# Kernel tuning notes

Hardware: AMD Instinct MI355X
Metric: run time of the kernel (lower is better)

## Reference

```python
import jax, jax.numpy as jnp
import numpy as np

B, T, D, HD = 4, 4096, 1024, 64

def setup_inputs() -> dict:
    key = jax.random.key(0)
    k1, k2, k3, k4 = jax.random.split(key, 4)
    scale = 1.0 / np.sqrt(D)
    return {
        "x": jax.random.normal(k1, (B, T, D), dtype=jnp.float32),
        "Wq": jax.random.normal(k2, (HD, D), dtype=jnp.float32) * scale,
        "Wk": jax.random.normal(k3, (HD, D), dtype=jnp.float32) * scale,
        "Wv": jax.random.normal(k4, (HD, D), dtype=jnp.float32) * scale,
    }

def reference(x, Wq, Wk, Wv):
    # x: [B,T,D]; W*: [head_dim, D] (torch Linear weight layout)
    Q = jnp.einsum('btd,hd->bth', x, Wq)  # [B,T,HD]
    K = jnp.einsum('btd,hd->bth', x, Wk)
    V = jnp.einsum('btd,hd->bth', x, Wv)
    hd = Q.shape[-1]
    scores = jnp.einsum('bqh,bkh->bqk', Q, K) * (hd ** -0.5)  # [B,T,T]
    t = scores.shape[1]
    causal = jnp.tril(jnp.ones((t, t), dtype=bool))
    scores = jnp.where(causal, scores, -jnp.inf)
    att = jax.nn.softmax(scores, axis=-1)
    return jnp.einsum('bqk,bkh->bqh', att, V)  # [B,T,HD]
```

## Files before the change

kernel.cpp:

```cpp
#include <hip/hip_runtime.h>
#include <stdint.h>

#define B_  4
#define T_  4096
#define D_  1024
#define HD_ 64
#define BT_ 16384

typedef short bf16x8 __attribute__((ext_vector_type(8)));
typedef float f32x4  __attribute__((ext_vector_type(4)));
typedef unsigned short u16;
typedef u16 u16x4 __attribute__((ext_vector_type(4)));

#define M0_ 8.0f

__device__ __forceinline__ u16 f2bf(float f) {
    union { float f; unsigned u; } v; v.f = f;
    unsigned r = (v.u + 0x7FFF + ((v.u >> 16) & 1)) >> 16;
    return (u16)r;
}
__device__ __forceinline__ float bf2f(u16 u) {
    union { unsigned u; float f; } v; v.u = ((unsigned)u) << 16;
    return v.f;
}

__device__ __forceinline__ int slot_base(int qt) {
    int a = qt >> 4, r = qt & 15;
    return qt + 8 * a * (a - 1) + a * r;
}

__global__ __launch_bounds__(256) void wconv_kernel(
    const float* __restrict__ wq, const float* __restrict__ wk,
    const float* __restrict__ wv, u16* __restrict__ wb)
{
    const int j   = blockIdx.x >> 5;
    const int off = (blockIdx.x & 31) * 2048 + threadIdx.x * 8;
    const float* src = (j == 0) ? wq : ((j == 1) ? wk : wv);
    f32x4 a0 = *(const f32x4*)(src + off);
    f32x4 a1 = *(const f32x4*)(src + off + 4);
    bf16x8 b;
    #pragma unroll
    for (int i = 0; i < 4; ++i) { b[i] = (short)f2bf(a0[i]); b[4 + i] = (short)f2bf(a1[i]); }
    *(bf16x8*)(wb + j * 65536 + off) = b;
}

__global__ __launch_bounds__(256) void qkv_kernel(
    const float* __restrict__ x, const u16* __restrict__ wb,
    u16* __restrict__ qs, u16* __restrict__ kss, u16* __restrict__ vssT)
{
    __shared__ __align__(16) u16 xt[32][72];
    __shared__ __align__(16) u16 wt[192][72];

    const int tid  = threadIdx.x;
    const int lane = tid & 63;
    const int w    = tid >> 6;
    const int quad = lane >> 4;
    const int l16  = lane & 15;
    const int row0 = blockIdx.x * 32;
    const int sp   = w >> 1;
    const int gh   = (w & 1) * 6;

    const int xrow = tid >> 3;
    const int xcg  = tid & 7;

    f32x4 acc[6];
    #pragma unroll
    for (int g = 0; g < 6; ++g) acc[g] = (f32x4)0.0f;

    f32x4 xa, xb;
    bf16x8 wr[6];
    {
        const float* xp = x + (size_t)(row0 + xrow) * D_ + xcg * 8;
        xa = *(const f32x4*)xp; xb = *(const f32x4*)(xp + 4);
        #pragma unroll
        for (int i = 0; i < 6; ++i) {
            int chunk = tid + 256 * i;
            wr[i] = *(const bf16x8*)(wb + (size_t)(chunk >> 3) * D_ + (chunk & 7) * 8);
        }
    }

    for (int kc = 0; kc < 16; ++kc) {
        __syncthreads();
        {
            bf16x8 px;
            #pragma unroll
            for (int i = 0; i < 4; ++i) { px[i] = (short)f2bf(xa[i]); px[4 + i] = (short)f2bf(xb[i]); }
            *(bf16x8*)&xt[xrow][xcg * 8] = px;
            #pragma unroll
            for (int i = 0; i < 6; ++i) {
                int chunk = tid + 256 * i;
                *(bf16x8*)&wt[chunk >> 3][(chunk & 7) * 8] = wr[i];
            }
        }
        __syncthreads();
        if (kc < 15) {
            const float* xp = x + (size_t)(row0 + xrow) * D_ + (kc + 1) * 64 + xcg * 8;
            xa = *(const f32x4*)xp; xb = *(const f32x4*)(xp + 4);
            #pragma unroll
            for (int i = 0; i < 6; ++i) {
                int chunk = tid + 256 * i;
                wr[i] = *(const bf16x8*)(wb + (size_t)(chunk >> 3) * D_ + (kc + 1) * 64 + (chunk & 7) * 8);
            }
        }
        #pragma unroll
        for (int ks = 0; ks < 2; ++ks) {
            bf16x8 a = *(const bf16x8*)&xt[sp * 16 + l16][ks * 32 + quad * 8];
            #pragma unroll
            for (int g = 0; g < 6; ++g) {
                bf16x8 b = *(const bf16x8*)&wt[(gh + g) * 16 + l16][ks * 32 + quad * 8];
                acc[g] = __builtin_amdgcn_mfma_f32_16x16x32_bf16(a, b, acc[g], 0, 0, 0);
            }
        }
    }
    #pragma unroll
    for (int g = 0; g < 6; ++g) {
        const int n = (gh + g) * 16 + l16;
        const int j = n >> 6, h = n & 63;
        const int rbase = row0 + sp * 16 + quad * 4;
        if (j == 0) {
            #pragma unroll
            for (int r = 0; r < 4; ++r) qs[(size_t)(rbase + r) * HD_ + h] = f2bf(acc[g][r] * 0.125f);
        } else if (j == 1) {
            #pragma unroll
            for (int r = 0; r < 4; ++r) kss[(size_t)(rbase + r) * HD_ + h] = f2bf(acc[g][r]);
        } else {
            u16x4 v;
            #pragma unroll
            for (int r = 0; r < 4; ++r) v[r] = f2bf(acc[g][r]);
            *(u16x4*)(vssT + (size_t)h * BT_ + rbase) = v;
        }
    }
}

__global__ __launch_bounds__(256) void attn_kernel(
    const u16* __restrict__ qs, const u16* __restrict__ kss,
    const u16* __restrict__ vssT,
    float* __restrict__ pl, u16* __restrict__ pO)
{
    __shared__ __align__(16) u16 kt[64][72];
    __shared__ __align__(16) u16 vt[80][72];
    __shared__ __align__(16) u16 pt[4][16][72];

    const int bi = blockIdx.x;
    const int c  = bi & 3;
    const int qt = (bi >> 2) & 63;
    const int b  = bi >> 8;
    if ((c << 4) > qt) return;

    const int kt0  = c << 4;
    const int kend = ((kt0 + 15) < qt) ? (kt0 + 15) : qt;

    const int tid  = threadIdx.x;
    const int lane = tid & 63;
    const int w    = tid >> 6;
    const int quad = lane >> 4;
    const int l16  = lane & 15;
    const int qb   = qt * 64;
    const size_t base = (size_t)b * T_;

    for (int idx = tid; idx < 16 * 72; idx += 256) {
        int rr = idx / 72, cc = idx - rr * 72;
        vt[64 + rr][cc] = (rr == 0) ? (u16)0x3F80 : (u16)0;
    }

    bf16x8 qf[2];
    {
        const u16* qp = qs + (base + qb + w * 16 + l16) * HD_ + quad * 8;
        qf[0] = *(const bf16x8*)(qp);
        qf[1] = *(const bf16x8*)(qp + 32);
    }

    f32x4 o_acc[5];
    #pragma unroll
    for (int g = 0; g < 5; ++g) o_acc[g] = (f32x4)0.0f;

    const int lr = tid >> 2, lp = tid & 3;

    bf16x8 kr0, kr1, vr0, vr1;
    {
        const u16* sk = kss + (base + kt0 * 64 + lr) * HD_ + lp * 16;
        kr0 = *(const bf16x8*)(sk);  kr1 = *(const bf16x8*)(sk + 8);
        const u16* sv = vssT + (size_t)lr * BT_ + base + kt0 * 64 + lp * 16;
        vr0 = *(const bf16x8*)(sv);  vr1 = *(const bf16x8*)(sv + 8);
    }

    for (int kti = kt0; kti <= kend; ++kti) {
        __syncthreads();
        *(bf16x8*)&kt[lr][lp * 16]     = kr0;
        *(bf16x8*)&kt[lr][lp * 16 + 8] = kr1;
        *(bf16x8*)&vt[lr][lp * 16]     = vr0;
        *(bf16x8*)&vt[lr][lp * 16 + 8] = vr1;
        __syncthreads();
        if (kti < kend) {
            const u16* sk = kss + (base + (kti + 1) * 64 + lr) * HD_ + lp * 16;
            kr0 = *(const bf16x8*)(sk);  kr1 = *(const bf16x8*)(sk + 8);
            const u16* sv = vssT + (size_t)lr * BT_ + base + (kti + 1) * 64 + lp * 16;
            vr0 = *(const bf16x8*)(sv);  vr1 = *(const bf16x8*)(sv + 8);
        }

        f32x4 s[4];
        #pragma unroll
        for (int g = 0; g < 4; ++g) {
            s[g] = (f32x4)0.0f;
            #pragma unroll
            for (int ks = 0; ks < 2; ++ks) {
                bf16x8 kf = *(const bf16x8*)&kt[g * 16 + l16][ks * 32 + quad * 8];
                s[g] = __builtin_amdgcn_mfma_f32_16x16x32_bf16(qf[ks], kf, s[g], 0, 0, 0);
            }
        }
        if (kti == qt) {
            #pragma unroll
            for (int g = 0; g < 4; ++g) {
                int key = kti * 64 + g * 16 + l16;
                #pragma unroll
                for (int r = 0; r < 4; ++r) {
                    int q = qb + w * 16 + quad * 4 + r;
                    if (key > q) s[g][r] = -1e30f;
                }
            }
        }
        #pragma unroll
        for (int g = 0; g < 4; ++g)
            #pragma unroll
            for (int r = 0; r < 4; ++r)
                pt[w][quad * 4 + r][g * 16 + l16] = f2bf(__expf(s[g][r] - M0_));
        #pragma unroll
        for (int ks = 0; ks < 2; ++ks) {
            bf16x8 pa = *(const bf16x8*)&pt[w][l16][ks * 32 + quad * 8];
            #pragma unroll
            for (int g = 0; g < 5; ++g) {
                bf16x8 vf = *(const bf16x8*)&vt[g * 16 + l16][ks * 32 + quad * 8];
                o_acc[g] = __builtin_amdgcn_mfma_f32_16x16x32_bf16(pa, vf, o_acc[g], 0, 0, 0);
            }
        }
    }

    const int slot = b * 160 + slot_base(qt) + c;
    if (l16 == 0) {
        #pragma unroll
        for (int r = 0; r < 4; ++r)
            pl[slot * 64 + w * 16 + quad * 4 + r] = o_acc[4][r];
    }
    #pragma unroll
    for (int g = 0; g < 4; ++g) {
        #pragma unroll
        for (int r = 0; r < 4; ++r) {
            int row = w * 16 + quad * 4 + r;
            pO[(size_t)slot * 4096 + row * 64 + g * 16 + l16] = f2bf(o_acc[g][r]);
        }
    }
}

__global__ __launch_bounds__(256) void merge_kernel(
    const float* __restrict__ pl, const u16* __restrict__ pO,
    float* __restrict__ out)
{
    const int bi = blockIdx.x;
    const int qt = bi & 63, b = bi >> 6;
    const int nc = (qt >> 4) + 1;
    const int s0 = b * 160 + slot_base(qt);
    const int row = threadIdx.x >> 2;
    const int hg  = (threadIdx.x & 3) * 16;

    float L = 0.0f;
    for (int c2 = 0; c2 < nc; ++c2) L += pl[(s0 + c2) * 64 + row];

    float o[16];
    #pragma unroll
    for (int i = 0; i < 16; ++i) o[i] = 0.0f;
    for (int c2 = 0; c2 < nc; ++c2) {
        const u16* p = pO + (size_t)(s0 + c2) * 4096 + row * 64 + hg;
        bf16x8 v0 = *(const bf16x8*)p;
        bf16x8 v1 = *(const bf16x8*)(p + 8);
        #pragma unroll
        for (int i = 0; i < 8; ++i) {
            o[i]     += bf2f((u16)v0[i]);
            o[8 + i] += bf2f((u16)v1[i]);
        }
    }
    const float inv = 1.0f / L;
    float* op = out + ((size_t)b * T_ + qt * 64 + row) * HD_ + hg;
    #pragma unroll
    for (int j = 0; j < 4; ++j) {
        f32x4 v;
        #pragma unroll
        for (int i = 0; i < 4; ++i) v[i] = o[j * 4 + i] * inv;
        *(f32x4*)(op + j * 4) = v;
    }
}

extern "C" void kernel_launch(void* const* d_in, const int* in_sizes, int n_in,
                              void* d_out, int out_size, void* d_ws, size_t ws_size,
                              hipStream_t stream) {
    const float* x  = (const float*)d_in[0];
    const float* wq = (const float*)d_in[1];
    const float* wk = (const float*)d_in[2];
    const float* wv = (const float*)d_in[3];

    const size_t NE = (size_t)BT_ * HD_;
    char* ws = (char*)d_ws;
    u16* qs   = (u16*)ws;
    u16* kss  = qs  + NE;
    u16* vssT = kss + NE;
    u16* wb   = vssT + NE;
    float* pl = (float*)(wb + 192 * 1024);
    u16* pO   = (u16*)(pl + 640 * 64);
    float* out = (float*)d_out;

    wconv_kernel<<<dim3(96),   dim3(256), 0, stream>>>(wq, wk, wv, wb);
    qkv_kernel  <<<dim3(512),  dim3(256), 0, stream>>>(x, wb, qs, kss, vssT);
    attn_kernel <<<dim3(1024), dim3(256), 0, stream>>>(qs, kss, vssT, pl, pO);
    merge_kernel<<<dim3(256),  dim3(256), 0, stream>>>(pl, pO, out);
}
```

Before: 152.2 us.

## Process two query tiles per attention block and double QKV k-chunk depth

```diff
diff --git a/kernel.cpp b/kernel.cpp
--- a/kernel.cpp
+++ b/kernel.cpp
@@ -24,9 +24,9 @@
     return v.f;
 }
 
-__device__ __forceinline__ int slot_base(int qt) {
-    int a = qt >> 4, r = qt & 15;
-    return qt + 8 * a * (a - 1) + a * r;
+__device__ __forceinline__ int slot_base(int Q) {
+    int a = Q >> 2, r = Q & 3;
+    return Q + 2 * a * (a - 1) + a * r;
 }
 
 __global__ __launch_bounds__(256) void wconv_kernel(
@@ -48,8 +48,8 @@
     const float* __restrict__ x, const u16* __restrict__ wb,
     u16* __restrict__ qs, u16* __restrict__ kss, u16* __restrict__ vssT)
 {
-    __shared__ __align__(16) u16 xt[32][72];
-    __shared__ __align__(16) u16 wt[192][72];
+    __shared__ __align__(16) u16 xt[32][136];
+    __shared__ __align__(16) u16 wt[192][136];
 
     const int tid  = threadIdx.x;
     const int lane = tid & 63;
@@ -67,43 +67,51 @@
     #pragma unroll
     for (int g = 0; g < 6; ++g) acc[g] = (f32x4)0.0f;
 
-    f32x4 xa, xb;
-    bf16x8 wr[6];
+    f32x4  xr[4];
+    bf16x8 wr[12];
     {
-        const float* xp = x + (size_t)(row0 + xrow) * D_ + xcg * 8;
-        xa = *(const f32x4*)xp; xb = *(const f32x4*)(xp + 4);
-        #pragma unroll
-        for (int i = 0; i < 6; ++i) {
+        const float* xp = x + (size_t)(row0 + xrow) * D_ + xcg * 16;
+        #pragma unroll
+        for (int i = 0; i < 4; ++i) xr[i] = *(const f32x4*)(xp + i * 4);
+        #pragma unroll
+        for (int i = 0; i < 12; ++i) {
             int chunk = tid + 256 * i;
-            wr[i] = *(const bf16x8*)(wb + (size_t)(chunk >> 3) * D_ + (chunk & 7) * 8);
-        }
-    }
-
-    for (int kc = 0; kc < 16; ++kc) {
+            wr[i] = *(const bf16x8*)(wb + (size_t)(chunk >> 4) * D_ + (chunk & 15) * 8);
+        }
+    }
+
+    for (int kc = 0; kc < 8; ++kc) {
         __syncthreads();
         {
-            bf16x8 px;
-            #pragma unroll
-            for (int i = 0; i < 4; ++i) { px[i] = (short)f2bf(xa[i]); px[4 + i] = (short)f2bf(xb[i]); }
-            *(bf16x8*)&xt[xrow][xcg * 8] = px;
-            #pragma unroll
-            for (int i = 0; i < 6; ++i) {
+            bf16x8 p0, p1;
+            #pragma unroll
+            for (int i = 0; i < 4; ++i) {
+                p0[i]     = (short)f2bf(xr[0][i]);
+                p0[4 + i] = (short)f2bf(xr[1][i]);
+                p1[i]     = (short)f2bf(xr[2][i]);
+                p1[4 + i] = (short)f2bf(xr[3][i]);
+            }
+            *(bf16x8*)&xt[xrow][xcg * 16]     = p0;
+            *(bf16x8*)&xt[xrow][xcg * 16 + 8] = p1;
+            #pragma unroll
+            for (int i = 0; i < 12; ++i) {
                 int chunk = tid + 256 * i;
-                *(bf16x8*)&wt[chunk >> 3][(chunk & 7) * 8] = wr[i];
+                *(bf16x8*)&wt[chunk >> 4][(chunk & 15) * 8] = wr[i];
             }
         }
         __syncthreads();
-        if (kc < 15) {
-            const float* xp = x + (size_t)(row0 + xrow) * D_ + (kc + 1) * 64 + xcg * 8;
-            xa = *(const f32x4*)xp; xb = *(const f32x4*)(xp + 4);
-            #pragma unroll
-            for (int i = 0; i < 6; ++i) {
+        if (kc < 7) {
+            const float* xp = x + (size_t)(row0 + xrow) * D_ + (kc + 1) * 128 + xcg * 16;
+            #pragma unroll
+            for (int i = 0; i < 4; ++i) xr[i] = *(const f32x4*)(xp + i * 4);
+            #pragma unroll
+            for (int i = 0; i < 12; ++i) {
                 int chunk = tid + 256 * i;
-                wr[i] = *(const bf16x8*)(wb + (size_t)(chunk >> 3) * D_ + (kc + 1) * 64 + (chunk & 7) * 8);
-            }
-        }
-        #pragma unroll
-        for (int ks = 0; ks < 2; ++ks) {
+                wr[i] = *(const bf16x8*)(wb + (size_t)(chunk >> 4) * D_ + (kc + 1) * 128 + (chunk & 15) * 8);
+            }
+        }
+        #pragma unroll
+        for (int ks = 0; ks < 4; ++ks) {
             bf16x8 a = *(const bf16x8*)&xt[sp * 16 + l16][ks * 32 + quad * 8];
             #pragma unroll
             for (int g = 0; g < 6; ++g) {
@@ -139,23 +147,22 @@
 {
     __shared__ __align__(16) u16 kt[64][72];
     __shared__ __align__(16) u16 vt[80][72];
-    __shared__ __align__(16) u16 pt[4][16][72];
+    __shared__ __align__(16) u16 pt[4][32][72];
 
     const int bi = blockIdx.x;
-    const int c  = bi & 3;
-    const int qt = (bi >> 2) & 63;
+    const int c  = bi & 7;
+    const int Q  = (bi >> 3) & 31;
     const int b  = bi >> 8;
-    if ((c << 4) > qt) return;
-
-    const int kt0  = c << 4;
-    const int kend = ((kt0 + 15) < qt) ? (kt0 + 15) : qt;
+    const int kt0 = c * 8;
+    if (kt0 > 2 * Q + 1) return;
+    const int kend = ((kt0 + 7) < (2 * Q + 1)) ? (kt0 + 7) : (2 * Q + 1);
 
     const int tid  = threadIdx.x;
     const int lane = tid & 63;
     const int w    = tid >> 6;
     const int quad = lane >> 4;
     const int l16  = lane & 15;
-    const int qb   = qt * 64;
+    const int qb   = Q * 128;
     const size_t base = (size_t)b * T_;
 
     for (int idx = tid; idx < 16 * 72; idx += 256) {
@@ -163,16 +170,19 @@
         vt[64 + rr][cc] = (rr == 0) ? (u16)0x3F80 : (u16)0;
     }
 
-    bf16x8 qf[2];
-    {
-        const u16* qp = qs + (base + qb + w * 16 + l16) * HD_ + quad * 8;
-        qf[0] = *(const bf16x8*)(qp);
-        qf[1] = *(const bf16x8*)(qp + 32);
-    }
-
-    f32x4 o_acc[5];
-    #pragma unroll
-    for (int g = 0; g < 5; ++g) o_acc[g] = (f32x4)0.0f;
+    bf16x8 qf[2][2];
+    #pragma unroll
+    for (int st = 0; st < 2; ++st) {
+        const u16* qp = qs + (base + qb + st * 64 + w * 16 + l16) * HD_ + quad * 8;
+        qf[st][0] = *(const bf16x8*)(qp);
+        qf[st][1] = *(const bf16x8*)(qp + 32);
+    }
+
+    f32x4 o_acc[2][5];
+    #pragma unroll
+    for (int st = 0; st < 2; ++st)
+        #pragma unroll
+        for (int g = 0; g < 5; ++g) o_acc[st][g] = (f32x4)0.0f;
 
     const int lr = tid >> 2, lp = tid & 3;
 
@@ -198,57 +208,64 @@
             vr0 = *(const bf16x8*)(sv);  vr1 = *(const bf16x8*)(sv + 8);
         }
 
-        f32x4 s[4];
-        #pragma unroll
-        for (int g = 0; g < 4; ++g) {
-            s[g] = (f32x4)0.0f;
+        #pragma unroll
+        for (int st = 0; st < 2; ++st) {
+            if (st == 0 && kti == 2 * Q + 1) continue;
+            f32x4 s[4];
+            #pragma unroll
+            for (int g = 0; g < 4; ++g) {
+                s[g] = (f32x4)0.0f;
+                #pragma unroll
+                for (int ks = 0; ks < 2; ++ks) {
+                    bf16x8 kf = *(const bf16x8*)&kt[g * 16 + l16][ks * 32 + quad * 8];
+                    s[g] = __builtin_amdgcn_mfma_f32_16x16x32_bf16(qf[st][ks], kf, s[g], 0, 0, 0);
+                }
+            }
+            if (kti == 2 * Q + st) {
+                #pragma unroll
+                for (int g = 0; g < 4; ++g) {
+                    int key = kti * 64 + g * 16 + l16;
+                    #pragma unroll
+                    for (int r = 0; r < 4; ++r) {
+                        int q = qb + st * 64 + w * 16 + quad * 4 + r;
+                        if (key > q) s[g][r] = -1e30f;
+                    }
+                }
+            }
+            #pragma unroll
+            for (int g = 0; g < 4; ++g)
+                #pragma unroll
+                for (int r = 0; r < 4; ++r)
+                    pt[w][st * 16 + quad * 4 + r][g * 16 + l16] = f2bf(__expf(s[g][r] - M0_));
             #pragma unroll
             for (int ks = 0; ks < 2; ++ks) {
-                bf16x8 kf = *(const bf16x8*)&kt[g * 16 + l16][ks * 32 + quad * 8];
-                s[g] = __builtin_amdgcn_mfma_f32_16x16x32_bf16(qf[ks], kf, s[g], 0, 0, 0);
-            }
-        }
-        if (kti == qt) {
-            #pragma unroll
-            for (int g = 0; g < 4; ++g) {
-                int key = kti * 64 + g * 16 + l16;
+                bf16x8 pa = *(const bf16x8*)&pt[w][st * 16 + l16][ks * 32 + quad * 8];
                 #pragma unroll
-                for (int r = 0; r < 4; ++r) {
-                    int q = qb + w * 16 + quad * 4 + r;
-                    if (key > q) s[g][r] = -1e30f;
+                for (int g = 0; g < 5; ++g) {
+                    bf16x8 vf = *(const bf16x8*)&vt[g * 16 + l16][ks * 32 + quad * 8];
+                    o_acc[st][g] = __builtin_amdgcn_mfma_f32_16x16x32_bf16(pa, vf, o_acc[st][g], 0, 0, 0);
                 }
             }
         }
+    }
+
+    const int slot = b * 144 + slot_base(Q) + c;
+    if (l16 == 0) {
+        #pragma unroll
+        for (int st = 0; st < 2; ++st)
+            #pragma unroll
+            for (int r = 0; r < 4; ++r)
+                pl[slot * 128 + st * 64 + w * 16 + quad * 4 + r] = o_acc[st][4][r];
+    }
+    #pragma unroll
+    for (int st = 0; st < 2; ++st)
         #pragma unroll
         for (int g = 0; g < 4; ++g)
             #pragma unroll
-            for (int r = 0; r < 4; ++r)
-                pt[w][quad * 4 + r][g * 16 + l16] = f2bf(__expf(s[g][r] - M0_));
-        #pragma unroll
-        for (int ks = 0; ks < 2; ++ks) {
-            bf16x8 pa = *(const bf16x8*)&pt[w][l16][ks * 32 + quad * 8];
-            #pragma unroll
-            for (int g = 0; g < 5; ++g) {
-                bf16x8 vf = *(const bf16x8*)&vt[g * 16 + l16][ks * 32 + quad * 8];
-                o_acc[g] = __builtin_amdgcn_mfma_f32_16x16x32_bf16(pa, vf, o_acc[g], 0, 0, 0);
-            }
-        }
-    }
-
-    const int slot = b * 160 + slot_base(qt) + c;
-    if (l16 == 0) {
-        #pragma unroll
-        for (int r = 0; r < 4; ++r)
-            pl[slot * 64 + w * 16 + quad * 4 + r] = o_acc[4][r];
-    }
-    #pragma unroll
-    for (int g = 0; g < 4; ++g) {
-        #pragma unroll
-        for (int r = 0; r < 4; ++r) {
-            int row = w * 16 + quad * 4 + r;
-            pO[(size_t)slot * 4096 + row * 64 + g * 16 + l16] = f2bf(o_acc[g][r]);
-        }
-    }
+            for (int r = 0; r < 4; ++r) {
+                int row = st * 64 + w * 16 + quad * 4 + r;
+                pO[(size_t)slot * 8192 + row * 64 + g * 16 + l16] = f2bf(o_acc[st][g][r]);
+            }
 }
 
 __global__ __launch_bounds__(256) void merge_kernel(
@@ -257,19 +274,21 @@
 {
     const int bi = blockIdx.x;
     const int qt = bi & 63, b = bi >> 6;
-    const int nc = (qt >> 4) + 1;
-    const int s0 = b * 160 + slot_base(qt);
+    const int Q = qt >> 1, half = qt & 1;
+    const int nc = ((qt | 1) >> 3) + 1;
+    const int s0 = b * 144 + slot_base(Q);
     const int row = threadIdx.x >> 2;
     const int hg  = (threadIdx.x & 3) * 16;
+    const int rowIn = half * 64 + row;
 
     float L = 0.0f;
-    for (int c2 = 0; c2 < nc; ++c2) L += pl[(s0 + c2) * 64 + row];
+    for (int c2 = 0; c2 < nc; ++c2) L += pl[(s0 + c2) * 128 + rowIn];
 
     float o[16];
     #pragma unroll
     for (int i = 0; i < 16; ++i) o[i] = 0.0f;
     for (int c2 = 0; c2 < nc; ++c2) {
-        const u16* p = pO + (size_t)(s0 + c2) * 4096 + row * 64 + hg;
+        const u16* p = pO + (size_t)(s0 + c2) * 8192 + rowIn * 64 + hg;
         bf16x8 v0 = *(const bf16x8*)p;
         bf16x8 v1 = *(const bf16x8*)(p + 8);
         #pragma unroll
@@ -304,7 +323,7 @@
     u16* vssT = kss + NE;
     u16* wb   = vssT + NE;
     float* pl = (float*)(wb + 192 * 1024);
-    u16* pO   = (u16*)(pl + 640 * 64);
+    u16* pO   = (u16*)(pl + 576 * 128);
     float* out = (float*)d_out;
 
     wconv_kernel<<<dim3(96),   dim3(256), 0, stream>>>(wq, wk, wv, wb);
```

Result: slower. 159.6 us (+4.8%).

## Halve QKV row tile and split attention KV into finer chunks

Applied to the files above, without the earlier changes.

```diff
diff --git a/kernel.cpp b/kernel.cpp
--- a/kernel.cpp
+++ b/kernel.cpp
@@ -25,8 +25,8 @@
 }
 
 __device__ __forceinline__ int slot_base(int qt) {
-    int a = qt >> 4, r = qt & 15;
-    return qt + 8 * a * (a - 1) + a * r;
+    int a = qt >> 3, r = qt & 7;
+    return (a + 1) * (4 * a + r);
 }
 
 __global__ __launch_bounds__(256) void wconv_kernel(
@@ -48,7 +48,7 @@
     const float* __restrict__ x, const u16* __restrict__ wb,
     u16* __restrict__ qs, u16* __restrict__ kss, u16* __restrict__ vssT)
 {
-    __shared__ __align__(16) u16 xt[32][72];
+    __shared__ __align__(16) u16 xt[16][72];
     __shared__ __align__(16) u16 wt[192][72];
 
     const int tid  = threadIdx.x;
@@ -56,22 +56,19 @@
     const int w    = tid >> 6;
     const int quad = lane >> 4;
     const int l16  = lane & 15;
-    const int row0 = blockIdx.x * 32;
-    const int sp   = w >> 1;
-    const int gh   = (w & 1) * 6;
-
-    const int xrow = tid >> 3;
-    const int xcg  = tid & 7;
-
-    f32x4 acc[6];
-    #pragma unroll
-    for (int g = 0; g < 6; ++g) acc[g] = (f32x4)0.0f;
-
-    f32x4 xa, xb;
+    const int row0 = blockIdx.x * 16;
+
+    const int xrow = tid >> 4;
+    const int xcg  = tid & 15;
+
+    f32x4 acc[3];
+    #pragma unroll
+    for (int g = 0; g < 3; ++g) acc[g] = (f32x4)0.0f;
+
+    f32x4  xr;
     bf16x8 wr[6];
     {
-        const float* xp = x + (size_t)(row0 + xrow) * D_ + xcg * 8;
-        xa = *(const f32x4*)xp; xb = *(const f32x4*)(xp + 4);
+        xr = *(const f32x4*)(x + (size_t)(row0 + xrow) * D_ + xcg * 4);
         #pragma unroll
         for (int i = 0; i < 6; ++i) {
             int chunk = tid + 256 * i;
@@ -82,10 +79,10 @@
     for (int kc = 0; kc < 16; ++kc) {
         __syncthreads();
         {
-            bf16x8 px;
-            #pragma unroll
-            for (int i = 0; i < 4; ++i) { px[i] = (short)f2bf(xa[i]); px[4 + i] = (short)f2bf(xb[i]); }
-            *(bf16x8*)&xt[xrow][xcg * 8] = px;
+            u16x4 px;
+            #pragma unroll
+            for (int i = 0; i < 4; ++i) px[i] = f2bf(xr[i]);
+            *(u16x4*)&xt[xrow][xcg * 4] = px;
             #pragma unroll
             for (int i = 0; i < 6; ++i) {
                 int chunk = tid + 256 * i;
@@ -94,8 +91,7 @@
         }
         __syncthreads();
         if (kc < 15) {
-            const float* xp = x + (size_t)(row0 + xrow) * D_ + (kc + 1) * 64 + xcg * 8;
-            xa = *(const f32x4*)xp; xb = *(const f32x4*)(xp + 4);
+            xr = *(const f32x4*)(x + (size_t)(row0 + xrow) * D_ + (kc + 1) * 64 + xcg * 4);
             #pragma unroll
             for (int i = 0; i < 6; ++i) {
                 int chunk = tid + 256 * i;
@@ -104,19 +100,19 @@
         }
         #pragma unroll
         for (int ks = 0; ks < 2; ++ks) {
-            bf16x8 a = *(const bf16x8*)&xt[sp * 16 + l16][ks * 32 + quad * 8];
-            #pragma unroll
-            for (int g = 0; g < 6; ++g) {
-                bf16x8 b = *(const bf16x8*)&wt[(gh + g) * 16 + l16][ks * 32 + quad * 8];
+            bf16x8 a = *(const bf16x8*)&xt[l16][ks * 32 + quad * 8];
+            #pragma unroll
+            for (int g = 0; g < 3; ++g) {
+                bf16x8 b = *(const bf16x8*)&wt[(w * 3 + g) * 16 + l16][ks * 32 + quad * 8];
                 acc[g] = __builtin_amdgcn_mfma_f32_16x16x32_bf16(a, b, acc[g], 0, 0, 0);
             }
         }
     }
     #pragma unroll
-    for (int g = 0; g < 6; ++g) {
-        const int n = (gh + g) * 16 + l16;
+    for (int g = 0; g < 3; ++g) {
+        const int n = (w * 3 + g) * 16 + l16;
         const int j = n >> 6, h = n & 63;
-        const int rbase = row0 + sp * 16 + quad * 4;
+        const int rbase = row0 + quad * 4;
         if (j == 0) {
             #pragma unroll
             for (int r = 0; r < 4; ++r) qs[(size_t)(rbase + r) * HD_ + h] = f2bf(acc[g][r] * 0.125f);
@@ -142,13 +138,12 @@
     __shared__ __align__(16) u16 pt[4][16][72];
 
     const int bi = blockIdx.x;
-    const int c  = bi & 3;
-    const int qt = (bi >> 2) & 63;
-    const int b  = bi >> 8;
-    if ((c << 4) > qt) return;
-
-    const int kt0  = c << 4;
-    const int kend = ((kt0 + 15) < qt) ? (kt0 + 15) : qt;
+    const int c  = bi & 7;
+    const int qt = (bi >> 3) & 63;
+    const int b  = bi >> 9;
+    const int kt0 = c * 8;
+    if (kt0 > qt) return;
+    const int kend = ((kt0 + 7) < qt) ? (kt0 + 7) : qt;
 
     const int tid  = threadIdx.x;
     const int lane = tid & 63;
@@ -235,7 +230,7 @@
         }
     }
 
-    const int slot = b * 160 + slot_base(qt) + c;
+    const int slot = b * 288 + slot_base(qt) + c;
     if (l16 == 0) {
         #pragma unroll
         for (int r = 0; r < 4; ++r)
@@ -257,8 +252,8 @@
 {
     const int bi = blockIdx.x;
     const int qt = bi & 63, b = bi >> 6;
-    const int nc = (qt >> 4) + 1;
-    const int s0 = b * 160 + slot_base(qt);
+    const int nc = (qt >> 3) + 1;
+    const int s0 = b * 288 + slot_base(qt);
     const int row = threadIdx.x >> 2;
     const int hg  = (threadIdx.x & 3) * 16;
 
@@ -304,11 +299,11 @@
     u16* vssT = kss + NE;
     u16* wb   = vssT + NE;
     float* pl = (float*)(wb + 192 * 1024);
-    u16* pO   = (u16*)(pl + 640 * 64);
+    u16* pO   = (u16*)(pl + 1152 * 64);
     float* out = (float*)d_out;
 
     wconv_kernel<<<dim3(96),   dim3(256), 0, stream>>>(wq, wk, wv, wb);
-    qkv_kernel  <<<dim3(512),  dim3(256), 0, stream>>>(x, wb, qs, kss, vssT);
-    attn_kernel <<<dim3(1024), dim3(256), 0, stream>>>(qs, kss, vssT, pl, pO);
+    qkv_kernel  <<<dim3(1024), dim3(256), 0, stream>>>(x, wb, qs, kss, vssT);
+    attn_kernel <<<dim3(2048), dim3(256), 0, stream>>>(qs, kss, vssT, pl, pO);
     merge_kernel<<<dim3(256),  dim3(256), 0, stream>>>(pl, pO, out);
 }
```

Result: slower. 167.9 us (+10.3%).
